# Performance work log

Hardware: AMD Instinct MI355X
Metric: run time of the kernel (lower is better)

## Reference

```python
import jax, jax.numpy as jnp
import numpy as np

EMBED_DIM = 256
NUM_HEADS = 8
HEAD_DIM = EMBED_DIM // NUM_HEADS
SCALING = HEAD_DIM ** -0.5
SEQ = 1024
BSZ = 4


def setup_inputs() -> dict:
    rng = jax.random.key(0)
    ks = jax.random.split(rng, 5)
    E = EMBED_DIM
    q = jax.random.normal(ks[0], (SEQ, BSZ, E), jnp.float32)
    k = jax.random.normal(ks[1], (SEQ, BSZ, E), jnp.float32)
    v = jax.random.normal(ks[2], (SEQ, BSZ, E), jnp.float32)
    # xavier-uniform-like scale for the packed 9E x E projection
    lim_in = np.sqrt(6.0 / (9 * E + E)).astype(np.float32)
    in_proj_w = jax.random.uniform(ks[3], (9 * E, E), jnp.float32, -lim_in, lim_in)
    in_proj_b = jnp.zeros((9 * E,), jnp.float32)
    lim_out = np.sqrt(6.0 / (E + E)).astype(np.float32)
    out_w = jax.random.uniform(ks[4], (E, E), jnp.float32, -lim_out, lim_out)
    out_b = jnp.zeros((E,), jnp.float32)
    return {"query": q, "key": k, "value": v,
            "in_proj_w": in_proj_w, "in_proj_b": in_proj_b,
            "out_w": out_w, "out_b": out_b,
            "shape0": 32, "shape1": 32}


def reference(query, key, value, in_proj_w, in_proj_b, out_w, out_b, shape0, shape1):
    S, B, E = query.shape
    H, hd = NUM_HEADS, HEAD_DIM

    def proj(x, i):  # slice i of the packed in-projection
        return x @ in_proj_w[i * E:(i + 1) * E].T + in_proj_b[i * E:(i + 1) * E]

    def heads(x):  # [S,B,E] -> [B*H, S, hd]
        return x.reshape(S, B * H, hd).transpose(1, 0, 2)

    q      = heads(proj(query, 0) * SCALING)
    k      = heads(proj(key, 1))
    v      = heads(proj(value, 2))
    q_left = heads(proj(query, 3))
    k_left = heads(proj(key, 4))
    q_right = heads(proj(query, 5))
    k_right = heads(proj(key, 6))
    q_loc  = heads(proj(query, 7) * SCALING)
    k_loc  = heads(proj(key, 8))

    global_w = q @ k.transpose(0, 2, 1)        # [BH,S,S]
    local_w  = q_loc @ k_loc.transpose(0, 2, 1)

    left_sm  = jax.nn.softmax(q_left @ k_left.transpose(0, 2, 1), axis=-1)
    right_sm = jax.nn.softmax(q_right @ k_right.transpose(0, 2, 1), axis=-1)

    triu = jnp.triu(jnp.ones((S, S), query.dtype))
    mini = jnp.tile(jnp.triu(jnp.ones((shape1, shape1), query.dtype)), (shape0, shape0))
    triu = (triu * mini)[None]                 # [1,S,S]
    triu_t = triu.transpose(0, 2, 1)

    fw_mask = (left_sm @ triu) * (right_sm @ triu_t)
    bw_mask = (left_sm @ triu_t) * (right_sm @ triu)
    local_mask = fw_mask + bw_mask             # [BH,S,S]

    attn_w = jax.nn.softmax(0.1 * global_w + local_w * local_mask, axis=-1)
    attn = (attn_w @ v).transpose(1, 0, 2).reshape(S, B, E)
    attn = attn @ out_w.T + out_b
    consistent_mask = local_mask.sum(axis=0)   # [S,S]
    return attn, consistent_mask
```

## Files before the change

kernel.cpp:

```cpp
#include <hip/hip_runtime.h>


typedef _Float16 v8h __attribute__((ext_vector_type(8)));
typedef _Float16 v4h __attribute__((ext_vector_type(4)));
typedef _Float16 v2h __attribute__((ext_vector_type(2)));
typedef float    v4f __attribute__((ext_vector_type(4)));

#define SL 1048576
#define RS 1032

static constexpr float SCALE = 0.17677669529663687f;


__global__ __launch_bounds__(256)
void cvt_kernel(const float* __restrict__ q, const float* __restrict__ k,
                const float* __restrict__ v, const float* __restrict__ W,
                _Float16* __restrict__ X16, _Float16* __restrict__ W16)
{
    const int b = blockIdx.x;
    const int t = threadIdx.x;
    const float* src; _Float16* dst; int off;
    if (b < 512)       { src = q; dst = X16;             off = b; }
    else if (b < 1024) { src = k; dst = X16 + (1 << 20); off = b - 512; }
    else if (b < 1536) { src = v; dst = X16 + (2 << 20); off = b - 1024; }
    else               { src = W; dst = W16;             off = b - 1536; }
    const int i = off * 2048 + t * 8;
    const float4 a = *(const float4*)(src + i);
    const float4 c = *(const float4*)(src + i + 4);
    v8h h;
    h[0] = (_Float16)a.x; h[1] = (_Float16)a.y; h[2] = (_Float16)a.z; h[3] = (_Float16)a.w;
    h[4] = (_Float16)c.x; h[5] = (_Float16)c.y; h[6] = (_Float16)c.z; h[7] = (_Float16)c.w;
    *(v8h*)(dst + i) = h;
}

__global__ __launch_bounds__(256)
void proj_kernel(const _Float16* __restrict__ X16, const _Float16* __restrict__ W16,
                 const float* __restrict__ bias, _Float16* __restrict__ P)
{
    const int t  = threadIdx.x;
    const int n0 = blockIdx.x * 64;
    const int m0 = blockIdx.y * 64;
    const int slice = n0 >> 8;
    const bool kslice = (slice == 1) || (slice == 4) || (slice == 6) || (slice == 8);
    const _Float16* X = X16 + (slice == 2 ? (2 << 20) : (kslice ? (1 << 20) : 0));
    const int w = t >> 6, lane = t & 63, m16 = lane & 15, kg = lane >> 4;
    const v4f zero = {0.f, 0.f, 0.f, 0.f};
    v4f acc[4] = {zero, zero, zero, zero};
    const _Float16* Arow = X + (size_t)(m0 + w * 16 + m16) * 256 + kg * 8;
    const _Float16* B0   = W16 + (size_t)(n0 + m16) * 256 + kg * 8;
#pragma unroll
    for (int kk = 0; kk < 8; ++kk) {
        const v8h a = *(const v8h*)(Arow + kk * 32);
#pragma unroll
        for (int nf = 0; nf < 4; ++nf) {
            const v8h bb = *(const v8h*)(B0 + nf * 4096 + kk * 32);
            acc[nf] = __builtin_amdgcn_mfma_f32_16x16x32_f16(a, bb, acc[nf], 0, 0, 0);
        }
    }
    const float scale = (slice == 0 || slice == 7) ? SCALE : 1.0f;
#pragma unroll
    for (int nf = 0; nf < 4; ++nf) {
        const int c = n0 + nf * 16 + m16;
        const float bv = bias[c];
        const int cc = c & 255;
        const int h = cc >> 5, d = cc & 31;
#pragma unroll
        for (int i = 0; i < 4; ++i) {
            const int m = m0 + w * 16 + kg * 4 + i;
            const int s = m >> 2, bs = m & 3;
            const int bh = bs * 8 + h;
            const float val = (acc[nf][i] + bv) * scale;
            size_t addr;
            if (slice == 2) {
                const int kc = s >> 5, kgv = (s >> 3) & 3, jj = s & 7;
                const int nt = d >> 4, nn = d & 15;
                addr = (size_t)2 * SL + (size_t)bh * 32768
                     + (size_t)((((kc << 1) + nt) << 6) + (nn + (kgv << 4))) * 8 + jj;
            } else {
                const int tile = s >> 4, mm = s & 15, kg8 = d >> 3, jj = d & 7;
                addr = (size_t)slice * SL + (size_t)bh * 32768
                     + (size_t)((tile << 6) + (mm + (kg8 << 4))) * 8 + jj;
            }
            P[addr] = (_Float16)val;
        }
    }
}

__global__ __launch_bounds__(512) __attribute__((amdgpu_waves_per_eu(4, 4)))
void attn_kernel(const _Float16* __restrict__ P, float* __restrict__ attn_pre,
                 _Float16* __restrict__ pmask)
{
    __shared__ __align__(16) _Float16 Lh[16 * RS];
    __shared__ __align__(16) _Float16 Rh[16 * RS];

    const int t    = threadIdx.x;
    const int bid  = blockIdx.x;
    const int q    = bid >> 3;
    const int bh   = ((bid & 7) << 2) + (q & 3);
    const int rt   = q >> 2;
    const int w    = __builtin_amdgcn_readfirstlane(t >> 6);
    const int lane = t & 63;
    const int m16  = lane & 15;
    const int kg   = lane >> 4;

    const _Float16* Pb = P + (size_t)bh * 32768;
    const v4f zero = {0.f, 0.f, 0.f, 0.f};

    {
        const v8h a_l = *(const v8h*)(Pb + 3 * SL + rt * 512 + lane * 8);
        const v8h a_r = *(const v8h*)(Pb + 5 * SL + rt * 512 + lane * 8);
        const _Float16* Bl = Pb + 4 * SL;
        const _Float16* Br = Pb + 6 * SL;
#pragma unroll 4
        for (int jt2 = 0; jt2 < 8; ++jt2) {
            const int jt = (w << 3) + jt2;
            const v8h bL = *(const v8h*)(Bl + jt * 512 + lane * 8);
            const v8h bR = *(const v8h*)(Br + jt * 512 + lane * 8);
            v4f cL = __builtin_amdgcn_mfma_f32_16x16x32_f16(a_l, bL, zero, 0, 0, 0);
            v4f cR = __builtin_amdgcn_mfma_f32_16x16x32_f16(a_r, bR, zero, 0, 0, 0);
            const int col = (jt << 4) + m16;
#pragma unroll
            for (int i = 0; i < 4; ++i) {
                Lh[((kg << 2) + i) * RS + col] = (_Float16)cL[i];
                Rh[((kg << 2) + i) * RS + col] = (_Float16)cR[i];
            }
        }
    }
    __syncthreads();

    auto softmax_pairs = [&](_Float16* ROW) {
        float v0[8], v1[8];
        float ss = 0.f;
#pragma unroll
        for (int kq = 0; kq < 8; ++kq) {
            const v2h pr = *(const v2h*)&ROW[(lane + (kq << 6)) << 1];
            v0[kq] = __expf((float)pr[0]);
            v1[kq] = __expf((float)pr[1]);
            ss += v0[kq] + v1[kq];
        }
#pragma unroll
        for (int off = 32; off; off >>= 1) ss += __shfl_xor(ss, off);
        const float inv = 1.f / ss;
#pragma unroll
        for (int kq = 0; kq < 8; ++kq) {
            v2h pr; pr[0] = (_Float16)(v0[kq] * inv); pr[1] = (_Float16)(v1[kq] * inv);
            *(v2h*)&ROW[(lane + (kq << 6)) << 1] = pr;
        }
    };
#pragma unroll
    for (int r = 0; r < 2; ++r) {
        softmax_pairs(&Lh[((w << 1) + r) * RS]);
        softmax_pairs(&Rh[((w << 1) + r) * RS]);
    }

    {
        const int kr = lane & 31;
#pragma unroll
        for (int r = 0; r < 2; ++r) {
            _Float16* ROW = (lane >= 32) ? &Rh[((w << 1) + r) * RS] : &Lh[((w << 1) + r) * RS];
            float run = 0.f;
#pragma unroll 4
            for (int kb = 0; kb < 32; ++kb) {
                float x = (float)ROW[(kb << 5) + kr];
#pragma unroll
                for (int off = 1; off < 32; off <<= 1) {
                    float y = __shfl_up(x, off, 32);
                    if (kr >= off) x += y;
                }
                run += x;
                ROW[(kb << 5) + kr] = (_Float16)run;
            }
        }
    }
    __syncthreads();

    v4h sc4[8];
    {
        _Float16* pm = pmask + (size_t)bh * 1048576 + (size_t)rt * 16384;
        const v8h a_g = *(const v8h*)(Pb + 0 * SL + rt * 512 + lane * 8);
        const v8h a_c = *(const v8h*)(Pb + 7 * SL + rt * 512 + lane * 8);
        const _Float16* Bg = Pb + 1 * SL;
        const _Float16* Bc = Pb + 8 * SL;
#pragma unroll
        for (int jt2 = 0; jt2 < 8; ++jt2) {
            const int jt  = (w << 3) + jt2;
            const int jb  = jt >> 1;
            const int jr  = ((jt & 1) << 4) + m16;
            const int col = (jt << 4) + m16;
            const v8h bG = *(const v8h*)(Bg + jt * 512 + lane * 8);
            const v8h bC = *(const v8h*)(Bc + jt * 512 + lane * 8);
            const v4f g4 = __builtin_amdgcn_mfma_f32_16x16x32_f16(a_g, bG, zero, 0, 0, 0);
            const v4f l4 = __builtin_amdgcn_mfma_f32_16x16x32_f16(a_c, bC, zero, 0, 0, 0);
            v4h s4, m4;
#pragma unroll
            for (int i = 0; i < 4; ++i) {
                const int rr = ((kg << 2) + i) * RS;
                const float PL  = (float)Lh[rr + col];
                const float PR  = (float)Rh[rr + col];
                const float eLb = jb ? (float)Lh[rr + (jb << 5) - 1] : 0.f;
                const float eRb = jb ? (float)Rh[rr + (jb << 5) - 1] : 0.f;
                const float eLc = jr ? (float)Lh[rr + 991 + jr] : 0.f;
                const float eRc = jr ? (float)Rh[rr + 991 + jr] : 0.f;
                const float eLbc = (jb && jr) ? (float)Lh[rr + ((jb - 1) << 5) + jr - 1] : 0.f;
                const float eRbc = (jb && jr) ? (float)Rh[rr + ((jb - 1) << 5) + jr - 1] : 0.f;
                const float SLv = 1.0f - eLb - eLc + eLbc;
                const float SRv = 1.0f - eRb - eRc + eRbc;
                const float mkv = PL * SRv + SLv * PR;
                s4[i] = (_Float16)(0.1f * g4[i] + l4[i] * mkv);
                m4[i] = (_Float16)mkv;
            }
            sc4[jt2] = s4;
            *(v4h*)(pm + ((size_t)jt << 8) + (lane << 2)) = m4;
        }
    }
    __syncthreads();

    {
#pragma unroll
        for (int jt2 = 0; jt2 < 8; ++jt2) {
            const int col = ((((w << 3) + jt2)) << 4) + m16;
#pragma unroll
            for (int i = 0; i < 4; ++i)
                Lh[((kg << 2) + i) * RS + col] = sc4[jt2][i];
        }
    }
    __syncthreads();

#pragma unroll
    for (int r = 0; r < 2; ++r) softmax_pairs(&Lh[((w << 1) + r) * RS]);
    __syncthreads();

    {
        const int nt = w & 1, hf = w >> 1;
        v4f c = zero;
        const _Float16* Vb = Pb + 2 * SL + nt * 512 + lane * 8;
        const int kc0 = hf << 3;
#pragma unroll 4
        for (int kc2 = 0; kc2 < 8; ++kc2) {
            const int kc = kc0 + kc2;
            const v8h a = *(const v8h*)&Lh[m16 * RS + (kc << 5) + (kg << 3)];
            const v8h b = *(const v8h*)(Vb + (size_t)kc * 1024);
            c = __builtin_amdgcn_mfma_f32_16x16x32_f16(a, b, c, 0, 0, 0);
        }
        float* Pbuf = (float*)&Rh[0];
#pragma unroll
        for (int i = 0; i < 4; ++i) Pbuf[(w << 8) + (lane << 2) + i] = c[i];
    }
    __syncthreads();

    {
        const float* Pbuf = (const float*)&Rh[0];
        const int r   = t >> 5;
        const int d   = t & 31;
        const int nt2 = d >> 4, n = d & 15;
        const int kg2 = r >> 2, i2 = r & 3;
        const int off = (kg2 << 6) + (n << 2) + i2;
        float v = 0.f;
#pragma unroll
        for (int hf = 0; hf < 4; ++hf)
            v += Pbuf[(((hf << 1) + nt2) << 8) + off];
        const int srow = (rt << 4) + r;
        attn_pre[((size_t)(srow * 4 + (bh >> 3))) * 256 + (bh & 7) * 32 + d] = v;
    }
}

__global__ __launch_bounds__(256)
void cmask_reduce_kernel(const _Float16* __restrict__ pmask, float* __restrict__ cmask)
{
    __shared__ __align__(16) float T4[4][16][132];
    const int rt = blockIdx.x, wh = blockIdx.y;
    const int t = threadIdx.x;
    const int wv = t >> 6;
    const int lane = t & 63, m16 = lane & 15, kg = lane >> 4;
    float acc[8][4] = {};
    const _Float16* base = pmask + (size_t)rt * 16384 + ((size_t)wh << 11) + (lane << 2)
                         + ((size_t)wv << 3) * 1048576;
    for (int bh = 0; bh < 8; ++bh) {
        const _Float16* p = base + (size_t)bh * 1048576;
#pragma unroll
        for (int jt2 = 0; jt2 < 8; ++jt2) {
            const v4h h4 = *(const v4h*)(p + (jt2 << 8));
#pragma unroll
            for (int i = 0; i < 4; ++i) acc[jt2][i] += (float)h4[i];
        }
    }
#pragma unroll
    for (int jt2 = 0; jt2 < 8; ++jt2)
#pragma unroll
        for (int i = 0; i < 4; ++i)
            T4[wv][(kg << 2) + i][(jt2 << 4) + m16] = acc[jt2][i];
    __syncthreads();
    const int row = t >> 4;
    const int c0  = (t & 15) << 3;
#pragma unroll
    for (int h = 0; h < 2; ++h) {
        const int c = c0 + (h << 2);
        const float4 s0 = *(const float4*)&T4[0][row][c];
        const float4 s1 = *(const float4*)&T4[1][row][c];
        const float4 s2 = *(const float4*)&T4[2][row][c];
        const float4 s3 = *(const float4*)&T4[3][row][c];
        const float4 o = make_float4(s0.x + s1.x + s2.x + s3.x,
                                     s0.y + s1.y + s2.y + s3.y,
                                     s0.z + s1.z + s2.z + s3.z,
                                     s0.w + s1.w + s2.w + s3.w);
        *(float4*)&cmask[((size_t)((rt << 4) + row) << 10) + (wh << 7) + c] = o;
    }
}

__global__ __launch_bounds__(256)
void outproj_kernel(const float* __restrict__ A, const float* __restrict__ W,
                    const float* __restrict__ bias, float* __restrict__ C)
{
    __shared__ float As[16][68];
    __shared__ float Bs[16][68];
    const int t  = threadIdx.x;
    const int n0 = blockIdx.x * 64;
    const int m0 = blockIdx.y * 64;
    const int tx = t & 15, ty = t >> 4;
    const int lm = t >> 2, lk = (t & 3) << 2;
    float acc[4][4] = {};
    for (int k0 = 0; k0 < 256; k0 += 16) {
        float4 av = *(const float4*)(A + (size_t)(m0 + lm) * 256 + k0 + lk);
        float4 bv = *(const float4*)(W + (size_t)(n0 + lm) * 256 + k0 + lk);
        As[lk + 0][lm] = av.x; As[lk + 1][lm] = av.y; As[lk + 2][lm] = av.z; As[lk + 3][lm] = av.w;
        Bs[lk + 0][lm] = bv.x; Bs[lk + 1][lm] = bv.y; Bs[lk + 2][lm] = bv.z; Bs[lk + 3][lm] = bv.w;
        __syncthreads();
#pragma unroll
        for (int kk = 0; kk < 16; ++kk) {
            float4 a4 = *(const float4*)&As[kk][ty << 2];
            float4 b4 = *(const float4*)&Bs[kk][tx << 2];
            float aa[4] = {a4.x, a4.y, a4.z, a4.w};
            float bb[4] = {b4.x, b4.y, b4.z, b4.w};
#pragma unroll
            for (int i = 0; i < 4; ++i)
#pragma unroll
                for (int j = 0; j < 4; ++j)
                    acc[i][j] = fmaf(aa[i], bb[j], acc[i][j]);
        }
        __syncthreads();
    }
#pragma unroll
    for (int i = 0; i < 4; ++i) {
        const int m  = m0 + (ty << 2) + i;
        const int c0 = n0 + (tx << 2);
        float4 o = make_float4(acc[i][0] + bias[c0 + 0], acc[i][1] + bias[c0 + 1],
                               acc[i][2] + bias[c0 + 2], acc[i][3] + bias[c0 + 3]);
        *(float4*)&C[(size_t)m * 256 + c0] = o;
    }
}

extern "C" void kernel_launch(void* const* d_in, const int* in_sizes, int n_in,
                              void* d_out, int out_size, void* d_ws, size_t ws_size,
                              hipStream_t stream)
{
    const float* q  = (const float*)d_in[0];
    const float* k  = (const float*)d_in[1];
    const float* v  = (const float*)d_in[2];
    const float* Wi = (const float*)d_in[3];
    const float* bi = (const float*)d_in[4];
    const float* Wo = (const float*)d_in[5];
    const float* bo = (const float*)d_in[6];

    float* out      = (float*)d_out;
    float* attn_out = out;
    float* cmask    = out + 1048576;

    _Float16* Ppack    = (_Float16*)d_ws;
    float*    attn_pre = (float*)((char*)d_ws + 18874368);
    _Float16* pmask    = (_Float16*)((char*)d_ws + 23068672);
    _Float16* X16      = (_Float16*)((char*)d_ws + 90177536);
    _Float16* W16      = (_Float16*)((char*)d_ws + 96468992);

    cvt_kernel<<<1824, 256, 0, stream>>>(q, k, v, Wi, X16, W16);
    proj_kernel<<<dim3(36, 64), 256, 0, stream>>>(X16, W16, bi, Ppack);
    attn_kernel<<<2048, 512, 0, stream>>>(Ppack, attn_pre, pmask);
    cmask_reduce_kernel<<<dim3(64, 8), 256, 0, stream>>>(pmask, cmask);
    outproj_kernel<<<dim3(4, 64), 256, 0, stream>>>(attn_pre, Wo, bo, attn_out);
}
```

Baseline: 293.3 us.

## Fuse fp16 conversion into projection and merge tail kernels into one launch

The separate fp32-to-fp16 conversion pass is removed; the projection kernel now loads fp32 inputs and weights directly and converts them in registers before the MFMA. The cmask reduction and output projection are combined into one kernel that dispatches on block index, which saves a launch and lets the two run concurrently. The attention kernel's register hint moves from a waves-per-EU bound to a fixed 128-VGPR cap. Projection blocks now read fp32, which doubles global load traffic and repeats conversion work across reused tiles, and the VGPR cap may cause spills.

```diff
diff --git a/kernel.cpp b/kernel.cpp
--- a/kernel.cpp
+++ b/kernel.cpp
@@ -13,28 +13,8 @@
 
 
 __global__ __launch_bounds__(256)
-void cvt_kernel(const float* __restrict__ q, const float* __restrict__ k,
-                const float* __restrict__ v, const float* __restrict__ W,
-                _Float16* __restrict__ X16, _Float16* __restrict__ W16)
-{
-    const int b = blockIdx.x;
-    const int t = threadIdx.x;
-    const float* src; _Float16* dst; int off;
-    if (b < 512)       { src = q; dst = X16;             off = b; }
-    else if (b < 1024) { src = k; dst = X16 + (1 << 20); off = b - 512; }
-    else if (b < 1536) { src = v; dst = X16 + (2 << 20); off = b - 1024; }
-    else               { src = W; dst = W16;             off = b - 1536; }
-    const int i = off * 2048 + t * 8;
-    const float4 a = *(const float4*)(src + i);
-    const float4 c = *(const float4*)(src + i + 4);
-    v8h h;
-    h[0] = (_Float16)a.x; h[1] = (_Float16)a.y; h[2] = (_Float16)a.z; h[3] = (_Float16)a.w;
-    h[4] = (_Float16)c.x; h[5] = (_Float16)c.y; h[6] = (_Float16)c.z; h[7] = (_Float16)c.w;
-    *(v8h*)(dst + i) = h;
-}
-
-__global__ __launch_bounds__(256)
-void proj_kernel(const _Float16* __restrict__ X16, const _Float16* __restrict__ W16,
+void proj_kernel(const float* __restrict__ Q, const float* __restrict__ K,
+                 const float* __restrict__ V, const float* __restrict__ W,
                  const float* __restrict__ bias, _Float16* __restrict__ P)
 {
     const int t  = threadIdx.x;
@@ -42,18 +22,26 @@
     const int m0 = blockIdx.y * 64;
     const int slice = n0 >> 8;
     const bool kslice = (slice == 1) || (slice == 4) || (slice == 6) || (slice == 8);
-    const _Float16* X = X16 + (slice == 2 ? (2 << 20) : (kslice ? (1 << 20) : 0));
+    const float* X = (slice == 2) ? V : (kslice ? K : Q);
     const int w = t >> 6, lane = t & 63, m16 = lane & 15, kg = lane >> 4;
     const v4f zero = {0.f, 0.f, 0.f, 0.f};
     v4f acc[4] = {zero, zero, zero, zero};
-    const _Float16* Arow = X + (size_t)(m0 + w * 16 + m16) * 256 + kg * 8;
-    const _Float16* B0   = W16 + (size_t)(n0 + m16) * 256 + kg * 8;
+    const float* Arow = X + (size_t)(m0 + w * 16 + m16) * 256 + kg * 8;
+    const float* B0   = W + (size_t)(n0 + m16) * 256 + kg * 8;
 #pragma unroll
     for (int kk = 0; kk < 8; ++kk) {
-        const v8h a = *(const v8h*)(Arow + kk * 32);
+        const float4 a0 = *(const float4*)(Arow + kk * 32);
+        const float4 a1 = *(const float4*)(Arow + kk * 32 + 4);
+        v8h a;
+        a[0] = (_Float16)a0.x; a[1] = (_Float16)a0.y; a[2] = (_Float16)a0.z; a[3] = (_Float16)a0.w;
+        a[4] = (_Float16)a1.x; a[5] = (_Float16)a1.y; a[6] = (_Float16)a1.z; a[7] = (_Float16)a1.w;
 #pragma unroll
         for (int nf = 0; nf < 4; ++nf) {
-            const v8h bb = *(const v8h*)(B0 + nf * 4096 + kk * 32);
+            const float4 b0 = *(const float4*)(B0 + nf * 4096 + kk * 32);
+            const float4 b1 = *(const float4*)(B0 + nf * 4096 + kk * 32 + 4);
+            v8h bb;
+            bb[0] = (_Float16)b0.x; bb[1] = (_Float16)b0.y; bb[2] = (_Float16)b0.z; bb[3] = (_Float16)b0.w;
+            bb[4] = (_Float16)b1.x; bb[5] = (_Float16)b1.y; bb[6] = (_Float16)b1.z; bb[7] = (_Float16)b1.w;
             acc[nf] = __builtin_amdgcn_mfma_f32_16x16x32_f16(a, bb, acc[nf], 0, 0, 0);
         }
     }
@@ -86,7 +74,8 @@
     }
 }
 
-__global__ __launch_bounds__(512) __attribute__((amdgpu_waves_per_eu(4, 4)))
+__global__ __launch_bounds__(512)
+__attribute__((amdgpu_num_vgpr(128)))
 void attn_kernel(const _Float16* __restrict__ P, float* __restrict__ attn_pre,
                  _Float16* __restrict__ pmask)
 {
@@ -265,87 +254,89 @@
 }
 
 __global__ __launch_bounds__(256)
-void cmask_reduce_kernel(const _Float16* __restrict__ pmask, float* __restrict__ cmask)
+void tail_kernel(const _Float16* __restrict__ pmask, float* __restrict__ cmask,
+                 const float* __restrict__ A, const float* __restrict__ W,
+                 const float* __restrict__ bias, float* __restrict__ C)
 {
-    __shared__ __align__(16) float T4[4][16][132];
-    const int rt = blockIdx.x, wh = blockIdx.y;
+    __shared__ __align__(16) float SMEM[4 * 16 * 132];
+    const int bid = blockIdx.x;
     const int t = threadIdx.x;
-    const int wv = t >> 6;
-    const int lane = t & 63, m16 = lane & 15, kg = lane >> 4;
-    float acc[8][4] = {};
-    const _Float16* base = pmask + (size_t)rt * 16384 + ((size_t)wh << 11) + (lane << 2)
-                         + ((size_t)wv << 3) * 1048576;
-    for (int bh = 0; bh < 8; ++bh) {
-        const _Float16* p = base + (size_t)bh * 1048576;
-#pragma unroll
-        for (int jt2 = 0; jt2 < 8; ++jt2) {
-            const v4h h4 = *(const v4h*)(p + (jt2 << 8));
-#pragma unroll
-            for (int i = 0; i < 4; ++i) acc[jt2][i] += (float)h4[i];
-        }
-    }
-#pragma unroll
-    for (int jt2 = 0; jt2 < 8; ++jt2)
-#pragma unroll
-        for (int i = 0; i < 4; ++i)
-            T4[wv][(kg << 2) + i][(jt2 << 4) + m16] = acc[jt2][i];
-    __syncthreads();
-    const int row = t >> 4;
-    const int c0  = (t & 15) << 3;
-#pragma unroll
-    for (int h = 0; h < 2; ++h) {
-        const int c = c0 + (h << 2);
-        const float4 s0 = *(const float4*)&T4[0][row][c];
-        const float4 s1 = *(const float4*)&T4[1][row][c];
-        const float4 s2 = *(const float4*)&T4[2][row][c];
-        const float4 s3 = *(const float4*)&T4[3][row][c];
-        const float4 o = make_float4(s0.x + s1.x + s2.x + s3.x,
-                                     s0.y + s1.y + s2.y + s3.y,
-                                     s0.z + s1.z + s2.z + s3.z,
-                                     s0.w + s1.w + s2.w + s3.w);
-        *(float4*)&cmask[((size_t)((rt << 4) + row) << 10) + (wh << 7) + c] = o;
-    }
-}
-
-__global__ __launch_bounds__(256)
-void outproj_kernel(const float* __restrict__ A, const float* __restrict__ W,
-                    const float* __restrict__ bias, float* __restrict__ C)
-{
-    __shared__ float As[16][68];
-    __shared__ float Bs[16][68];
-    const int t  = threadIdx.x;
-    const int n0 = blockIdx.x * 64;
-    const int m0 = blockIdx.y * 64;
-    const int tx = t & 15, ty = t >> 4;
-    const int lm = t >> 2, lk = (t & 3) << 2;
-    float acc[4][4] = {};
-    for (int k0 = 0; k0 < 256; k0 += 16) {
-        float4 av = *(const float4*)(A + (size_t)(m0 + lm) * 256 + k0 + lk);
-        float4 bv = *(const float4*)(W + (size_t)(n0 + lm) * 256 + k0 + lk);
-        As[lk + 0][lm] = av.x; As[lk + 1][lm] = av.y; As[lk + 2][lm] = av.z; As[lk + 3][lm] = av.w;
-        Bs[lk + 0][lm] = bv.x; Bs[lk + 1][lm] = bv.y; Bs[lk + 2][lm] = bv.z; Bs[lk + 3][lm] = bv.w;
+
+    if (bid >= 256) {
+        const int b2 = bid - 256;
+        const int rt = b2 >> 3, wh = b2 & 7;
+        float (*T4)[16][132] = (float(*)[16][132])SMEM;
+        const int wv = t >> 6;
+        const int lane = t & 63, m16 = lane & 15, kg = lane >> 4;
+        float acc[8][4] = {};
+        const _Float16* base = pmask + (size_t)rt * 16384 + ((size_t)wh << 11) + (lane << 2)
+                             + ((size_t)wv << 3) * 1048576;
+        for (int bh = 0; bh < 8; ++bh) {
+            const _Float16* p = base + (size_t)bh * 1048576;
+#pragma unroll
+            for (int jt2 = 0; jt2 < 8; ++jt2) {
+                const v4h h4 = *(const v4h*)(p + (jt2 << 8));
+#pragma unroll
+                for (int i = 0; i < 4; ++i) acc[jt2][i] += (float)h4[i];
+            }
+        }
+#pragma unroll
+        for (int jt2 = 0; jt2 < 8; ++jt2)
+#pragma unroll
+            for (int i = 0; i < 4; ++i)
+                T4[wv][(kg << 2) + i][(jt2 << 4) + m16] = acc[jt2][i];
         __syncthreads();
-#pragma unroll
-        for (int kk = 0; kk < 16; ++kk) {
-            float4 a4 = *(const float4*)&As[kk][ty << 2];
-            float4 b4 = *(const float4*)&Bs[kk][tx << 2];
-            float aa[4] = {a4.x, a4.y, a4.z, a4.w};
-            float bb[4] = {b4.x, b4.y, b4.z, b4.w};
-#pragma unroll
-            for (int i = 0; i < 4; ++i)
-#pragma unroll
-                for (int j = 0; j < 4; ++j)
-                    acc[i][j] = fmaf(aa[i], bb[j], acc[i][j]);
-        }
-        __syncthreads();
-    }
-#pragma unroll
-    for (int i = 0; i < 4; ++i) {
-        const int m  = m0 + (ty << 2) + i;
-        const int c0 = n0 + (tx << 2);
-        float4 o = make_float4(acc[i][0] + bias[c0 + 0], acc[i][1] + bias[c0 + 1],
-                               acc[i][2] + bias[c0 + 2], acc[i][3] + bias[c0 + 3]);
-        *(float4*)&C[(size_t)m * 256 + c0] = o;
+        const int row = t >> 4;
+        const int c0  = (t & 15) << 3;
+#pragma unroll
+        for (int h = 0; h < 2; ++h) {
+            const int c = c0 + (h << 2);
+            const float4 s0 = *(const float4*)&T4[0][row][c];
+            const float4 s1 = *(const float4*)&T4[1][row][c];
+            const float4 s2 = *(const float4*)&T4[2][row][c];
+            const float4 s3 = *(const float4*)&T4[3][row][c];
+            const float4 o = make_float4(s0.x + s1.x + s2.x + s3.x,
+                                         s0.y + s1.y + s2.y + s3.y,
+                                         s0.z + s1.z + s2.z + s3.z,
+                                         s0.w + s1.w + s2.w + s3.w);
+            *(float4*)&cmask[((size_t)((rt << 4) + row) << 10) + (wh << 7) + c] = o;
+        }
+    } else {
+        const int n0 = (bid & 3) * 64;
+        const int m0 = (bid >> 2) * 64;
+        float (*As)[68] = (float(*)[68])SMEM;
+        float (*Bs)[68] = (float(*)[68])(SMEM + 16 * 68);
+        const int tx = t & 15, ty = t >> 4;
+        const int lm = t >> 2, lk = (t & 3) << 2;
+        float acc[4][4] = {};
+        for (int k0 = 0; k0 < 256; k0 += 16) {
+            float4 av = *(const float4*)(A + (size_t)(m0 + lm) * 256 + k0 + lk);
+            float4 bv = *(const float4*)(W + (size_t)(n0 + lm) * 256 + k0 + lk);
+            As[lk + 0][lm] = av.x; As[lk + 1][lm] = av.y; As[lk + 2][lm] = av.z; As[lk + 3][lm] = av.w;
+            Bs[lk + 0][lm] = bv.x; Bs[lk + 1][lm] = bv.y; Bs[lk + 2][lm] = bv.z; Bs[lk + 3][lm] = bv.w;
+            __syncthreads();
+#pragma unroll
+            for (int kk = 0; kk < 16; ++kk) {
+                float4 a4 = *(const float4*)&As[kk][ty << 2];
+                float4 b4 = *(const float4*)&Bs[kk][tx << 2];
+                float aa[4] = {a4.x, a4.y, a4.z, a4.w};
+                float bb[4] = {b4.x, b4.y, b4.z, b4.w};
+#pragma unroll
+                for (int i = 0; i < 4; ++i)
+#pragma unroll
+                    for (int j = 0; j < 4; ++j)
+                        acc[i][j] = fmaf(aa[i], bb[j], acc[i][j]);
+            }
+            __syncthreads();
+        }
+#pragma unroll
+        for (int i = 0; i < 4; ++i) {
+            const int m  = m0 + (ty << 2) + i;
+            const int c0 = n0 + (tx << 2);
+            float4 o = make_float4(acc[i][0] + bias[c0 + 0], acc[i][1] + bias[c0 + 1],
+                                   acc[i][2] + bias[c0 + 2], acc[i][3] + bias[c0 + 3]);
+            *(float4*)&C[(size_t)m * 256 + c0] = o;
+        }
     }
 }
 
@@ -368,12 +359,8 @@
     _Float16* Ppack    = (_Float16*)d_ws;
     float*    attn_pre = (float*)((char*)d_ws + 18874368);
     _Float16* pmask    = (_Float16*)((char*)d_ws + 23068672);
-    _Float16* X16      = (_Float16*)((char*)d_ws + 90177536);
-    _Float16* W16      = (_Float16*)((char*)d_ws + 96468992);
-
-    cvt_kernel<<<1824, 256, 0, stream>>>(q, k, v, Wi, X16, W16);
-    proj_kernel<<<dim3(36, 64), 256, 0, stream>>>(X16, W16, bi, Ppack);
+
+    proj_kernel<<<dim3(36, 64), 256, 0, stream>>>(q, k, v, Wi, bi, Ppack);
     attn_kernel<<<2048, 512, 0, stream>>>(Ppack, attn_pre, pmask);
-    cmask_reduce_kernel<<<dim3(64, 8), 256, 0, stream>>>(pmask, cmask);
-    outproj_kernel<<<dim3(4, 64), 256, 0, stream>>>(attn_pre, Wo, bo, attn_out);
+    tail_kernel<<<768, 256, 0, stream>>>(pmask, cmask, attn_pre, Wo, bo, attn_out);
 }
```

Result: slower. 349.3 us (+19.1%).

## Stage projection stores through LDS and merge cmask reduce with out-projection

Applied to the files above, without the earlier changes.

The projection epilogue now writes results into a shared-memory staging tile and then emits coalesced 16-byte vector stores in the packed attention layout, in place of scattered 2-byte global stores. The cmask reduction and out-projection kernels are combined into one launch that picks its role by block index, which removes one kernel launch and lets both run concurrently. The attention kernel's launch bounds are changed from a waves-per-EU attribute to a min-blocks hint. A stray label is left in the host code, which is legal C++ but unused.

```diff
diff --git a/kernel.cpp b/kernel.cpp
--- a/kernel.cpp
+++ b/kernel.cpp
@@ -37,10 +37,12 @@
 void proj_kernel(const _Float16* __restrict__ X16, const _Float16* __restrict__ W16,
                  const float* __restrict__ bias, _Float16* __restrict__ P)
 {
+    __shared__ __align__(16) _Float16 stage[4096];
     const int t  = threadIdx.x;
     const int n0 = blockIdx.x * 64;
     const int m0 = blockIdx.y * 64;
     const int slice = n0 >> 8;
+    const int q2 = (n0 >> 6) & 3;
     const bool kslice = (slice == 1) || (slice == 4) || (slice == 6) || (slice == 8);
     const _Float16* X = X16 + (slice == 2 ? (2 << 20) : (kslice ? (1 << 20) : 0));
     const int w = t >> 6, lane = t & 63, m16 = lane & 15, kg = lane >> 4;
@@ -62,31 +64,44 @@
     for (int nf = 0; nf < 4; ++nf) {
         const int c = n0 + nf * 16 + m16;
         const float bv = bias[c];
-        const int cc = c & 255;
-        const int h = cc >> 5, d = cc & 31;
 #pragma unroll
         for (int i = 0; i < 4; ++i) {
-            const int m = m0 + w * 16 + kg * 4 + i;
-            const int s = m >> 2, bs = m & 3;
-            const int bh = bs * 8 + h;
-            const float val = (acc[nf][i] + bv) * scale;
-            size_t addr;
+            const _Float16 val = (_Float16)((acc[nf][i] + bv) * scale);
+            const int lb = i * 2 + (nf >> 1);
+            int inner;
             if (slice == 2) {
-                const int kc = s >> 5, kgv = (s >> 3) & 3, jj = s & 7;
-                const int nt = d >> 4, nn = d & 15;
-                addr = (size_t)2 * SL + (size_t)bh * 32768
-                     + (size_t)((((kc << 1) + nt) << 6) + (nn + (kgv << 4))) * 8 + jj;
+                const int ls = w * 4 + kg;
+                inner = ((nf & 1) << 8) + ((ls >> 3) << 7) + m16 * 8 + (ls & 7);
             } else {
-                const int tile = s >> 4, mm = s & 15, kg8 = d >> 3, jj = d & 7;
-                addr = (size_t)slice * SL + (size_t)bh * 32768
-                     + (size_t)((tile << 6) + (mm + (kg8 << 4))) * 8 + jj;
-            }
-            P[addr] = (_Float16)val;
-        }
-    }
-}
-
-__global__ __launch_bounds__(512) __attribute__((amdgpu_waves_per_eu(4, 4)))
+                inner = ((w * 4 + kg) + (((nf & 1) * 2 + (m16 >> 3)) << 4)) * 8 + (m16 & 7);
+            }
+            stage[lb * 512 + inner] = val;
+        }
+    }
+    __syncthreads();
+    {
+        const int o  = t * 16;
+        const int lb = o >> 9;
+        const int inner = o & 511;
+        const int bs = lb >> 1, hh = lb & 1;
+        const int bh = bs * 8 + 2 * q2 + hh;
+        size_t dst;
+        if (slice == 2) {
+            const int kc = m0 >> 7;
+            const int g0 = (m0 >> 5) & 3;
+            const int nt = inner >> 8, a = (inner >> 7) & 1, r = inner & 127;
+            dst = (size_t)2 * SL + (size_t)bh * 32768
+                + (size_t)(kc * 1024 + nt * 512 + (g0 + a) * 128 + r);
+        } else {
+            const int tile = m0 >> 6;
+            dst = (size_t)slice * SL + (size_t)bh * 32768 + (size_t)(tile * 512 + inner);
+        }
+        *(v8h*)(P + dst)     = *(const v8h*)(stage + o);
+        *(v8h*)(P + dst + 8) = *(const v8h*)(stage + o + 8);
+    }
+}
+
+__global__ __launch_bounds__(512, 4)
 void attn_kernel(const _Float16* __restrict__ P, float* __restrict__ attn_pre,
                  _Float16* __restrict__ pmask)
 {
@@ -265,87 +280,89 @@
 }
 
 __global__ __launch_bounds__(256)
-void cmask_reduce_kernel(const _Float16* __restrict__ pmask, float* __restrict__ cmask)
-{
-    __shared__ __align__(16) float T4[4][16][132];
-    const int rt = blockIdx.x, wh = blockIdx.y;
+void tail_kernel(const _Float16* __restrict__ pmask, float* __restrict__ cmask,
+                 const float* __restrict__ A, const float* __restrict__ W,
+                 const float* __restrict__ bias, float* __restrict__ C)
+{
+    __shared__ __align__(16) float SMEM[4 * 16 * 132];
+    const int bid = blockIdx.x;
     const int t = threadIdx.x;
-    const int wv = t >> 6;
-    const int lane = t & 63, m16 = lane & 15, kg = lane >> 4;
-    float acc[8][4] = {};
-    const _Float16* base = pmask + (size_t)rt * 16384 + ((size_t)wh << 11) + (lane << 2)
-                         + ((size_t)wv << 3) * 1048576;
-    for (int bh = 0; bh < 8; ++bh) {
-        const _Float16* p = base + (size_t)bh * 1048576;
-#pragma unroll
-        for (int jt2 = 0; jt2 < 8; ++jt2) {
-            const v4h h4 = *(const v4h*)(p + (jt2 << 8));
-#pragma unroll
-            for (int i = 0; i < 4; ++i) acc[jt2][i] += (float)h4[i];
-        }
-    }
-#pragma unroll
-    for (int jt2 = 0; jt2 < 8; ++jt2)
-#pragma unroll
-        for (int i = 0; i < 4; ++i)
-            T4[wv][(kg << 2) + i][(jt2 << 4) + m16] = acc[jt2][i];
-    __syncthreads();
-    const int row = t >> 4;
-    const int c0  = (t & 15) << 3;
-#pragma unroll
-    for (int h = 0; h < 2; ++h) {
-        const int c = c0 + (h << 2);
-        const float4 s0 = *(const float4*)&T4[0][row][c];
-        const float4 s1 = *(const float4*)&T4[1][row][c];
-        const float4 s2 = *(const float4*)&T4[2][row][c];
-        const float4 s3 = *(const float4*)&T4[3][row][c];
-        const float4 o = make_float4(s0.x + s1.x + s2.x + s3.x,
-                                     s0.y + s1.y + s2.y + s3.y,
-                                     s0.z + s1.z + s2.z + s3.z,
-                                     s0.w + s1.w + s2.w + s3.w);
-        *(float4*)&cmask[((size_t)((rt << 4) + row) << 10) + (wh << 7) + c] = o;
-    }
-}
-
-__global__ __launch_bounds__(256)
-void outproj_kernel(const float* __restrict__ A, const float* __restrict__ W,
-                    const float* __restrict__ bias, float* __restrict__ C)
-{
-    __shared__ float As[16][68];
-    __shared__ float Bs[16][68];
-    const int t  = threadIdx.x;
-    const int n0 = blockIdx.x * 64;
-    const int m0 = blockIdx.y * 64;
-    const int tx = t & 15, ty = t >> 4;
-    const int lm = t >> 2, lk = (t & 3) << 2;
-    float acc[4][4] = {};
-    for (int k0 = 0; k0 < 256; k0 += 16) {
-        float4 av = *(const float4*)(A + (size_t)(m0 + lm) * 256 + k0 + lk);
-        float4 bv = *(const float4*)(W + (size_t)(n0 + lm) * 256 + k0 + lk);
-        As[lk + 0][lm] = av.x; As[lk + 1][lm] = av.y; As[lk + 2][lm] = av.z; As[lk + 3][lm] = av.w;
-        Bs[lk + 0][lm] = bv.x; Bs[lk + 1][lm] = bv.y; Bs[lk + 2][lm] = bv.z; Bs[lk + 3][lm] = bv.w;
+
+    if (bid >= 256) {
+        const int b2 = bid - 256;
+        const int rt = b2 >> 3, wh = b2 & 7;
+        float (*T4)[16][132] = (float(*)[16][132])SMEM;
+        const int wv = t >> 6;
+        const int lane = t & 63, m16 = lane & 15, kg = lane >> 4;
+        float acc[8][4] = {};
+        const _Float16* base = pmask + (size_t)rt * 16384 + ((size_t)wh << 11) + (lane << 2)
+                             + ((size_t)wv << 3) * 1048576;
+        for (int bh = 0; bh < 8; ++bh) {
+            const _Float16* p = base + (size_t)bh * 1048576;
+#pragma unroll
+            for (int jt2 = 0; jt2 < 8; ++jt2) {
+                const v4h h4 = *(const v4h*)(p + (jt2 << 8));
+#pragma unroll
+                for (int i = 0; i < 4; ++i) acc[jt2][i] += (float)h4[i];
+            }
+        }
+#pragma unroll
+        for (int jt2 = 0; jt2 < 8; ++jt2)
+#pragma unroll
+            for (int i = 0; i < 4; ++i)
+                T4[wv][(kg << 2) + i][(jt2 << 4) + m16] = acc[jt2][i];
         __syncthreads();
-#pragma unroll
-        for (int kk = 0; kk < 16; ++kk) {
-            float4 a4 = *(const float4*)&As[kk][ty << 2];
-            float4 b4 = *(const float4*)&Bs[kk][tx << 2];
-            float aa[4] = {a4.x, a4.y, a4.z, a4.w};
-            float bb[4] = {b4.x, b4.y, b4.z, b4.w};
-#pragma unroll
-            for (int i = 0; i < 4; ++i)
-#pragma unroll
-                for (int j = 0; j < 4; ++j)
-                    acc[i][j] = fmaf(aa[i], bb[j], acc[i][j]);
-        }
-        __syncthreads();
-    }
-#pragma unroll
-    for (int i = 0; i < 4; ++i) {
-        const int m  = m0 + (ty << 2) + i;
-        const int c0 = n0 + (tx << 2);
-        float4 o = make_float4(acc[i][0] + bias[c0 + 0], acc[i][1] + bias[c0 + 1],
-                               acc[i][2] + bias[c0 + 2], acc[i][3] + bias[c0 + 3]);
-        *(float4*)&C[(size_t)m * 256 + c0] = o;
+        const int row = t >> 4;
+        const int c0  = (t & 15) << 3;
+#pragma unroll
+        for (int h = 0; h < 2; ++h) {
+            const int c = c0 + (h << 2);
+            const float4 s0 = *(const float4*)&T4[0][row][c];
+            const float4 s1 = *(const float4*)&T4[1][row][c];
+            const float4 s2 = *(const float4*)&T4[2][row][c];
+            const float4 s3 = *(const float4*)&T4[3][row][c];
+            const float4 o = make_float4(s0.x + s1.x + s2.x + s3.x,
+                                         s0.y + s1.y + s2.y + s3.y,
+                                         s0.z + s1.z + s2.z + s3.z,
+                                         s0.w + s1.w + s2.w + s3.w);
+            *(float4*)&cmask[((size_t)((rt << 4) + row) << 10) + (wh << 7) + c] = o;
+        }
+    } else {
+        const int n0 = (bid & 3) * 64;
+        const int m0 = (bid >> 2) * 64;
+        float (*As)[68] = (float(*)[68])SMEM;
+        float (*Bs)[68] = (float(*)[68])(SMEM + 16 * 68);
+        const int tx = t & 15, ty = t >> 4;
+        const int lm = t >> 2, lk = (t & 3) << 2;
+        float acc[4][4] = {};
+        for (int k0 = 0; k0 < 256; k0 += 16) {
+            float4 av = *(const float4*)(A + (size_t)(m0 + lm) * 256 + k0 + lk);
+            float4 bv = *(const float4*)(W + (size_t)(n0 + lm) * 256 + k0 + lk);
+            As[lk + 0][lm] = av.x; As[lk + 1][lm] = av.y; As[lk + 2][lm] = av.z; As[lk + 3][lm] = av.w;
+            Bs[lk + 0][lm] = bv.x; Bs[lk + 1][lm] = bv.y; Bs[lk + 2][lm] = bv.z; Bs[lk + 3][lm] = bv.w;
+            __syncthreads();
+#pragma unroll
+            for (int kk = 0; kk < 16; ++kk) {
+                float4 a4 = *(const float4*)&As[kk][ty << 2];
+                float4 b4 = *(const float4*)&Bs[kk][tx << 2];
+                float aa[4] = {a4.x, a4.y, a4.z, a4.w};
+                float bb[4] = {b4.x, b4.y, b4.z, b4.w};
+#pragma unroll
+                for (int i = 0; i < 4; ++i)
+#pragma unroll
+                    for (int j = 0; j < 4; ++j)
+                        acc[i][j] = fmaf(aa[i], bb[j], acc[i][j]);
+            }
+            __syncthreads();
+        }
+#pragma unroll
+        for (int i = 0; i < 4; ++i) {
+            const int m  = m0 + (ty << 2) + i;
+            const int c0 = n0 + (tx << 2);
+            float4 o = make_float4(acc[i][0] + bias[c0 + 0], acc[i][1] + bias[c0 + 1],
+                                   acc[i][2] + bias[c0 + 2], acc[i][3] + bias[c0 + 3]);
+            *(float4*)&C[(size_t)m * 256 + c0] = o;
+        }
     }
 }
 
@@ -374,6 +391,6 @@
     cvt_kernel<<<1824, 256, 0, stream>>>(q, k, v, Wi, X16, W16);
     proj_kernel<<<dim3(36, 64), 256, 0, stream>>>(X16, W16, bi, Ppack);
     attn_kernel<<<2048, 512, 0, stream>>>(Ppack, attn_pre, pmask);
-    cmask_reduce_kernel<<<dim3(64, 8), 256, 0, stream>>>(pmask, cmask);
-    outproj_kernel<<<dim3(4, 64), 256, 0, stream>>>(attn_pre, Wo, bo, attn_out);
-}
+    cmask_reduce_kernel_dummy:;
+    tail_kernel<<<768, 256, 0, stream>>>(pmask, cmask, attn_pre, Wo, bo, attn_out);
+}
```

Measured after the change: 288.9 us. No clear change (-1.5%).
